# Performance work log

Hardware: AMD Instinct MI355X
Metric: run time of the kernel (lower is better)

The kernel has to match this reference:

```python
import jax, jax.numpy as jnp
import numpy as np

CONF_THRES = 0.2   # from __init__ default
IOU_THRES = 0.6    # from __init__ default
MAX_WH = 4096.0    # class-offset for multi-class NMS (yolov7 convention)
TOPK = 2048        # pre-NMS candidates per image
MAX_DET = 300      # max detections per image (yolov7 default)
B, N, NC = 8, 25200, 80


def setup_inputs() -> dict:
    key = jax.random.key(0)
    k1, k2, k3 = jax.random.split(key, 3)
    # decoded predictions: [cx, cy, w, h, obj, cls_0..cls_79]
    xywh = jax.random.uniform(k1, (B, N, 4)) * jnp.array([640.0, 640.0, 120.0, 120.0])
    obj = jax.random.uniform(k2, (B, N, 1))
    cls = jax.random.uniform(k3, (B, N, NC))
    preds = jnp.concatenate([xywh, obj, cls], axis=-1)  # [B, N, 85]
    return {"preds": preds}


def _xywh2xyxy(xywh):
    cx, cy, w, h = xywh[..., 0], xywh[..., 1], xywh[..., 2], xywh[..., 3]
    return jnp.stack([cx - w * 0.5, cy - h * 0.5, cx + w * 0.5, cy + h * 0.5], axis=-1)


def _box_iou(a, b):
    # a: [K,4], b: [K,4] -> [K,K] pairwise IoU
    area_a = (a[:, 2] - a[:, 0]) * (a[:, 3] - a[:, 1])
    area_b = (b[:, 2] - b[:, 0]) * (b[:, 3] - b[:, 1])
    lt = jnp.maximum(a[:, None, :2], b[None, :, :2])  # [K,K,2]
    rb = jnp.minimum(a[:, None, 2:], b[None, :, 2:])
    wh = jnp.clip(rb - lt, 0.0)
    inter = wh[..., 0] * wh[..., 1]
    return inter / (area_a[:, None] + area_b[None, :] - inter + 1e-9)


def _nms_single(pred):
    # pred: [N, 5+NC]
    boxes = _xywh2xyxy(pred[:, :4])                 # [N,4]
    scores_all = pred[:, 5:] * pred[:, 4:5]         # obj * cls  [N,NC]
    conf = jnp.max(scores_all, axis=-1)             # best-class conf
    cls_id = jnp.argmax(scores_all, axis=-1)
    scores = jnp.where(conf > CONF_THRES, conf, 0.0)

    # pre-NMS top-k candidates (sorted descending)
    top_scores, idx = jax.lax.top_k(scores, TOPK)
    top_boxes = boxes[idx]                          # [K,4]
    top_cls = cls_id[idx]                           # [K]
    top_valid = top_scores > CONF_THRES

    # per-class NMS via class offset so cross-class boxes never overlap
    offset_boxes = top_boxes + (top_cls.astype(top_boxes.dtype) * MAX_WH)[:, None]
    iou = _box_iou(offset_boxes, offset_boxes)      # [K,K]

    # greedy NMS over score-sorted candidates
    def body(i, state):
        keep, suppressed = state
        k_i = top_valid[i] & jnp.logical_not(suppressed[i])
        keep = keep.at[i].set(k_i)
        sup_new = suppressed | (k_i & (iou[i] > IOU_THRES))
        sup_new = sup_new.at[i].set(suppressed[i])  # never self-suppress
        return keep, sup_new

    keep, _ = jax.lax.fori_loop(
        0, TOPK, body,
        (jnp.zeros(TOPK, dtype=bool), jnp.zeros(TOPK, dtype=bool)))

    # take top MAX_DET kept detections
    keep_scores = jnp.where(keep, top_scores, -1.0)
    det_scores, det_idx = jax.lax.top_k(keep_scores, MAX_DET)
    det = jnp.concatenate(
        [top_boxes[det_idx],
         det_scores[:, None],
         top_cls[det_idx].astype(pred.dtype)[:, None]], axis=-1)  # [MAX_DET,6]
    det = jnp.where((det_scores > 0.0)[:, None], det, 0.0)
    return det


def reference(preds):
    # preds: [B, N, 5+NC] -> [B, MAX_DET, 6] (x1,y1,x2,y2,conf,cls), zero-padded
    return jax.vmap(_nms_single)(preds)
```

## Files before the change

### kernel.cpp

```cpp
#include <hip/hip_runtime.h>

#define BATCH 8
#define NPRED 25200
#define NCLS 80
#define ROWW 85
#define TOPKK 2048
#define MAXDET 300
#define CANDMAX 4096
#define NBUCKET 4096
#define CONF_T 0.2f
#define IOU_T 0.6f
#define CLS_OFF 4096.0f

#define MASKN 384
#define MCH (MASKN / 64)
#define MW 13

typedef unsigned long long u64;
typedef unsigned int u32;

__device__ __forceinline__ int bucket_of_key(u64 k) {
    float sc = __uint_as_float((u32)(k >> 32));
    int bkt = (int)(sc * (float)NBUCKET);
    return (bkt > NBUCKET - 1) ? (NBUCKET - 1) : bkt;
}

__global__ __launch_bounds__(256) void k_score(
    const float* __restrict__ preds,
    u64* __restrict__ keys,
    unsigned char* __restrict__ cls8)
{
    __shared__ float4 rows4[64 * ROWW / 4 + 4];
    const int t = threadIdx.x;
    const int lane = t & 63;
    const int wave = t >> 6;
    const size_t rowbase = (size_t)blockIdx.x * 64;
    const float4* src = reinterpret_cast<const float4*>(preds + rowbase * ROWW);

    for (int q = wave; q < 21; q += 4) {
        __builtin_amdgcn_global_load_lds(
            (const __attribute__((address_space(1))) void*)(src + q * 64 + lane),
            (__attribute__((address_space(3))) void*)(rows4 + q * 64),
            16, 0, 0);
    }
    if (t < 16) rows4[1344 + t] = src[1344 + t];
    __syncthreads();

    const float* rows = reinterpret_cast<const float*>(rows4);
    const int r = t >> 2;
    const int j = t & 3;
    const float* p = rows + r * ROWW;
    const float obj = p[4];

    float best = -1.0f;
    int bi = 0;
    #pragma unroll
    for (int tt = 0; tt < 20; ++tt) {
        int c = j + 4 * tt;
        float s = __fmul_rn(obj, p[5 + c]);
        if (s > best) { best = s; bi = c; }
    }
    #pragma unroll
    for (int d = 1; d <= 2; d <<= 1) {
        float os = __shfl_xor(best, d);
        int oi = __shfl_xor(bi, d);
        if (os > best || (os == best && oi < bi)) { best = os; bi = oi; }
    }

    if (j == 0) {
        unsigned gid = (unsigned)rowbase + r;
        u64 key = 0ull;
        if (best > CONF_T) {
            key = ((u64)__float_as_uint(best) << 32) | (0xFFFFFFFFu - (gid % NPRED));
        }
        keys[gid] = key;
        cls8[gid] = (unsigned char)bi;
    }
}

__global__ __launch_bounds__(1024) void k_scan(
    const u64* __restrict__ keys,
    u32* __restrict__ bstart_g,
    u32* __restrict__ balloc_g,
    int* __restrict__ tb_g,
    u32* __restrict__ stored_g)
{
    __shared__ u32 histL[NBUCKET];
    __shared__ u32 wtot[16];
    __shared__ u32 wsuf[16];
    __shared__ int s_tb;
    __shared__ u32 s_stored;

    const int b = blockIdx.x;
    const int t = threadIdx.x;
    const int lane = t & 63;
    const int wave = t >> 6;

    for (int i = t; i < NBUCKET; i += 1024) histL[i] = 0u;
    __syncthreads();

    const uint4* k4 = reinterpret_cast<const uint4*>(keys + (size_t)b * NPRED);
    for (int i = t; i < NPRED / 2; i += 1024) {
        uint4 v = k4[i];
        u64 ka = ((u64)v.y << 32) | v.x;
        u64 kb = ((u64)v.w << 32) | v.z;
        if (ka) atomicAdd(&histL[bucket_of_key(ka)], 1u);
        if (kb) atomicAdd(&histL[bucket_of_key(kb)], 1u);
    }
    __syncthreads();

    u32 h0 = histL[4 * t], h1 = histL[4 * t + 1], h2 = histL[4 * t + 2], h3 = histL[4 * t + 3];
    u32 ps = h0 + h1 + h2 + h3;

    u32 v = ps;
    #pragma unroll
    for (int off = 1; off < 64; off <<= 1) {
        u32 u2 = __shfl_down(v, off);
        if (lane + off < 64) v += u2;
    }
    if (lane == 0) wtot[wave] = v;
    __syncthreads();
    if (t < 16) {
        u32 w = wtot[t];
        u32 s = w;
        #pragma unroll
        for (int off = 1; off < 16; off <<= 1) {
            u32 u2 = __shfl_down(s, off);
            if (t + off < 16) s += u2;
        }
        wsuf[t] = s - w;
    }
    if (t == 0) s_tb = 0;
    __syncthreads();
    u32 suffix_t = v + wsuf[wave];
    u32 snext = suffix_t - ps;

    u32 b3 = snext;
    u32 b2 = b3 + h3;
    u32 b1 = b2 + h2;
    u32 b0 = b1 + h1;
    const size_t B0 = (size_t)b * NBUCKET;
    bstart_g[B0 + 4 * t + 0] = b0;
    bstart_g[B0 + 4 * t + 1] = b1;
    bstart_g[B0 + 4 * t + 2] = b2;
    bstart_g[B0 + 4 * t + 3] = b3;
    balloc_g[B0 + 4 * t + 0] = b0;
    balloc_g[B0 + 4 * t + 1] = b1;
    balloc_g[B0 + 4 * t + 2] = b2;
    balloc_g[B0 + 4 * t + 3] = b3;

    if (t == 0) s_stored = (suffix_t < (u32)CANDMAX) ? suffix_t : (u32)CANDMAX;
    __syncthreads();
    {
        u32 c3 = b3 + h3, c2 = b2 + h2, c1 = b1 + h1, c0 = b0 + h0;
        if (c3 >= TOPKK && b3 < TOPKK) { s_tb = 4 * t + 3; s_stored = (c3 < (u32)CANDMAX) ? c3 : (u32)CANDMAX; }
        if (c2 >= TOPKK && b2 < TOPKK) { s_tb = 4 * t + 2; s_stored = (c2 < (u32)CANDMAX) ? c2 : (u32)CANDMAX; }
        if (c1 >= TOPKK && b1 < TOPKK) { s_tb = 4 * t + 1; s_stored = (c1 < (u32)CANDMAX) ? c1 : (u32)CANDMAX; }
        if (c0 >= TOPKK && b0 < TOPKK) { s_tb = 4 * t + 0; s_stored = (c0 < (u32)CANDMAX) ? c0 : (u32)CANDMAX; }
    }
    __syncthreads();
    if (t == 0) { tb_g[b] = s_tb; stored_g[b] = s_stored; }
}

__global__ __launch_bounds__(256) void k_compact(
    const u64* __restrict__ keys,
    u32* __restrict__ balloc_g,
    const int* __restrict__ tb_g,
    u64* __restrict__ cand_g)
{
    unsigned i2 = blockIdx.x * 256 + threadIdx.x;
    if (i2 >= BATCH * NPRED / 2) return;
    uint4 v = reinterpret_cast<const uint4*>(keys)[i2];
    int b = (int)(i2 / (NPRED / 2));
    int tb = tb_g[b];
    u64 ka = ((u64)v.y << 32) | v.x;
    u64 kb = ((u64)v.w << 32) | v.z;
    if (ka) {
        int bkt = bucket_of_key(ka);
        if (bkt >= tb) {
            u32 slot = atomicAdd(&balloc_g[(size_t)b * NBUCKET + bkt], 1u);
            if (slot < CANDMAX) cand_g[(size_t)b * CANDMAX + slot] = ka;
        }
    }
    if (kb) {
        int bkt = bucket_of_key(kb);
        if (bkt >= tb) {
            u32 slot = atomicAdd(&balloc_g[(size_t)b * NBUCKET + bkt], 1u);
            if (slot < CANDMAX) cand_g[(size_t)b * CANDMAX + slot] = kb;
        }
    }
}

struct RankPhase {
    u32 bstartL[NBUCKET];
};
struct NmsPhase {
    u32 masks32[MASKN * MW];
    float4 cbx[MASKN];
    float carea[MASKN];
    float4 kb[MAXDET];
};

__global__ __launch_bounds__(1024) void k_finish(
    const float* __restrict__ preds,
    const unsigned char* __restrict__ cls8,
    const u32* __restrict__ bstart_g,
    const int* __restrict__ tb_g,
    const u32* __restrict__ stored_g,
    const u64* __restrict__ cand_g,
    float* __restrict__ out)
{
    __shared__ union { RankPhase rk; NmsPhase nms; } u;
    __shared__ u64 candL[CANDMAX];
    __shared__ unsigned short rank2cand[TOPKK];
    __shared__ float4 sbox[MASKN];
    __shared__ float sscore[MASKN];
    __shared__ float scls[MASKN];
    __shared__ u64 validw[MCH];

    const int b = blockIdx.x;
    const int t = threadIdx.x;
    const int lane = t & 63;
    const int wave = t >> 6;
    float* ob = out + (size_t)b * MAXDET * 6;
    const u32 stored = stored_g[b];
    const int tb = tb_g[b];
    const int tb2 = (tb > 0) ? tb - 1 : 0;

    for (int i = tb2 + t; i < NBUCKET; i += 1024)
        u.rk.bstartL[i] = bstart_g[(size_t)b * NBUCKET + i];
    for (int i = t; i < TOPKK; i += 1024) rank2cand[i] = 0xFFFFu;
    for (int i = t; i < CANDMAX; i += 1024)
        if ((u32)i < stored) candL[i] = cand_g[(size_t)b * CANDMAX + i];
    if (t < MASKN) {
        sbox[t] = make_float4(0.f, 0.f, 0.f, 0.f);
        sscore[t] = 0.f;
        scls[t] = 0.f;
    }
    __syncthreads();

    for (u32 i = t; i < stored; i += 1024) {
        u64 k = candL[i];
        int bkt = bucket_of_key(k);
        u32 base = u.rk.bstartL[bkt];
        u32 end = (bkt == 0) ? stored : u.rk.bstartL[bkt - 1];
        if (end > stored) end = stored;
        u32 r = base;
        for (u32 jx = base; jx < end; ++jx) r += (candL[jx] > k) ? 1u : 0u;
        if (r < TOPKK) rank2cand[r] = (unsigned short)i;
        if (r < MASKN) {
            float sc = __uint_as_float((u32)(k >> 32));
            unsigned idx = 0xFFFFFFFFu - (u32)(k & 0xFFFFFFFFu);
            const float* p = preds + ((size_t)b * NPRED + idx) * ROWW;
            float cx = p[0], cy = p[1], w = p[2], h = p[3];
            float hw = __fmul_rn(w, 0.5f);
            float hh = __fmul_rn(h, 0.5f);
            sbox[r] = make_float4(__fsub_rn(cx, hw), __fsub_rn(cy, hh),
                                  __fadd_rn(cx, hw), __fadd_rn(cy, hh));
            sscore[r] = sc;
            scls[r] = (float)cls8[(size_t)b * NPRED + idx];
        }
    }
    __syncthreads();

    if (t < MASKN) {
        float sc = sscore[t];
        float cl = scls[t];
        float4 bb = sbox[t];
        float off = __fmul_rn(cl, CLS_OFF);
        float4 obx = make_float4(__fadd_rn(bb.x, off), __fadd_rn(bb.y, off),
                                 __fadd_rn(bb.z, off), __fadd_rn(bb.w, off));
        u.nms.cbx[t] = obx;
        u.nms.carea[t] = __fmul_rn(__fsub_rn(obx.z, obx.x), __fsub_rn(obx.w, obx.y));
        u64 vb = __ballot(sc > CONF_T);
        if (lane == 0) validw[wave] = vb;
    }
    __syncthreads();

    for (int tu = 0; tu < 3; ++tu) {
        int uidx = wave + 16 * tu;
        if (uidx >= 42) break;
        int q, s;
        if (uidx < 12)      { q = 0; s = uidx; }
        else if (uidx < 22) { q = 1; s = uidx - 12 + 2; }
        else if (uidx < 30) { q = 2; s = uidx - 22 + 4; }
        else if (uidx < 36) { q = 3; s = uidx - 30 + 6; }
        else if (uidx < 40) { q = 4; s = uidx - 36 + 8; }
        else                { q = 5; s = uidx - 40 + 10; }

        const int r = q * 64 + lane;
        const float4 me = u.nms.cbx[r];
        const float aA = u.nms.carea[r];
        const int j0 = s * 32;
        u32 acc = 0u;
        #pragma unroll 8
        for (int jj = 0; jj < 32; ++jj) {
            const int jx = j0 + jj;
            float4 cb = u.nms.cbx[jx];
            float lx = fmaxf(me.x, cb.x), ly = fmaxf(me.y, cb.y);
            float rx = fminf(me.z, cb.z), ry = fminf(me.w, cb.w);
            float iw = fmaxf(__fsub_rn(rx, lx), 0.0f);
            float ih = fmaxf(__fsub_rn(ry, ly), 0.0f);
            float inter = __fmul_rn(iw, ih);
            float denom = __fadd_rn(__fsub_rn(__fadd_rn(aA, u.nms.carea[jx]), inter), 1e-9f);
            bool sv = inter > __fmul_rn(IOU_T, denom);
            acc |= ((u32)sv) << jj;
        }
        if (s == 2 * q || s == 2 * q + 1) {
            int shift = r - j0;
            u32 dm = (shift < 0) ? ~0u : ((shift >= 31) ? 0u : (~0u << (shift + 1)));
            acc &= dm;
        }
        u.nms.masks32[r * MW + s] = acc;
    }
    __syncthreads();
    if (wave != 0) return;

    const u64 below = (lane == 0) ? 0ull : (~0ull >> (64 - lane));
    u64 S[MCH];
    #pragma unroll
    for (int w = 0; w < MCH; ++w) S[w] = 0ull;
    int nk = 0;
    bool done = false, allfull = true;

    #pragma unroll
    for (int c = 0; c < MCH; ++c) {
        if (done) break;
        u64 vw = validw[c];
        u64 eligible = vw & ~S[c];
        const int rbase = (c * 64 + lane) * MW;
        u64 Mu = ((u64)u.nms.masks32[rbase + 2 * c + 1] << 32) |
                 (u64)u.nms.masks32[rbase + 2 * c];
        bool elig = (eligible >> lane) & 1ull;
        if (eligible) {
            int cap = MAXDET - nk;
            u64 edge = __ballot(elig && ((Mu & eligible) != 0ull));
            u64 keptm;
            if (edge == 0ull) {
                int rank = __popcll(eligible & below);
                keptm = __ballot(elig && (rank < cap));
            } else {
                u64 km = 0ull, supm = 0ull;
                int cnt = 0;
                for (int m = 0; m < 64 && cnt < cap; ++m) {
                    if (!((eligible >> m) & 1ull)) continue;
                    if ((supm >> m) & 1ull) continue;
                    km |= 1ull << m;
                    ++cnt;
                    supm |= __shfl(Mu, m);
                }
                keptm = km;
            }
            if ((keptm >> lane) & 1ull) {
                int pos = nk + __popcll(keptm & below);
                int i = c * 64 + lane;
                float4 bb = sbox[i];
                u.nms.kb[pos] = u.nms.cbx[i];
                float* row = ob + pos * 6;
                row[0] = bb.x; row[1] = bb.y; row[2] = bb.z; row[3] = bb.w;
                row[4] = sscore[i]; row[5] = scls[i];
            }
            nk += __popcll(keptm);
            if (nk >= MAXDET) {
                done = true;
            } else if (keptm) {
                for (int w = c + 1; w < MCH; ++w) {
                    u64 v2 = ((keptm >> lane) & 1ull)
                        ? (((u64)u.nms.masks32[rbase + 2 * w + 1] << 32) |
                           (u64)u.nms.masks32[rbase + 2 * w])
                        : 0ull;
                    v2 |= __shfl_xor(v2, 1);  v2 |= __shfl_xor(v2, 2);
                    v2 |= __shfl_xor(v2, 4);  v2 |= __shfl_xor(v2, 8);
                    v2 |= __shfl_xor(v2, 16); v2 |= __shfl_xor(v2, 32);
                    S[w] |= v2;
                }
            }
        }
        if (vw != ~0ull) { allfull = false; break; }
    }

    if (!done && allfull && nk < MAXDET) {
        __threadfence_block();
        for (int c = MCH; c < TOPKK / 64; ++c) {
            int r = c * 64 + lane;
            unsigned short ci = rank2cand[r];
            bool valid = (ci != 0xFFFFu);
            u64 validmask = __ballot(valid);
            if (validmask == 0ull) break;

            float sc = 0.f, cl = 0.f;
            float bx1 = 0.f, by1 = 0.f, bx2 = 0.f, by2 = 0.f;
            if (valid) {
                u64 k = candL[ci];
                sc = __uint_as_float((u32)(k >> 32));
                unsigned idx = 0xFFFFFFFFu - (u32)(k & 0xFFFFFFFFu);
                const float* p = preds + ((size_t)b * NPRED + idx) * ROWW;
                float cx = p[0], cy = p[1], w = p[2], h = p[3];
                float hw = __fmul_rn(w, 0.5f);
                float hh = __fmul_rn(h, 0.5f);
                bx1 = __fsub_rn(cx, hw); by1 = __fsub_rn(cy, hh);
                bx2 = __fadd_rn(cx, hw); by2 = __fadd_rn(cy, hh);
                cl = (float)cls8[(size_t)b * NPRED + idx];
            }
            float off = __fmul_rn(cl, CLS_OFF);
            float x1 = __fadd_rn(bx1, off), y1 = __fadd_rn(by1, off);
            float x2 = __fadd_rn(bx2, off), y2 = __fadd_rn(by2, off);
            float areaA = __fmul_rn(__fsub_rn(x2, x1), __fsub_rn(y2, y1));

            bool sup = false;
            for (int jx = 0; jx < nk; ++jx) {
                float4 k4 = u.nms.kb[jx];
                float lx = fmaxf(x1, k4.x), ly = fmaxf(y1, k4.y);
                float rx = fminf(x2, k4.z), ry = fminf(y2, k4.w);
                float iw = fmaxf(__fsub_rn(rx, lx), 0.0f);
                float ih = fmaxf(__fsub_rn(ry, ly), 0.0f);
                float inter = __fmul_rn(iw, ih);
                float areaB = __fmul_rn(__fsub_rn(k4.z, k4.x), __fsub_rn(k4.w, k4.y));
                float denom = __fadd_rn(__fsub_rn(__fadd_rn(areaA, areaB), inter), 1e-9f);
                if (inter > __fmul_rn(IOU_T, denom)) sup = true;
            }
            u64 supprev = __ballot(sup);

            u32 sb_lo = 0u, sb_hi = 0u;
            for (int m = 0; m < 64; ++m) {
                float mx1 = __shfl(x1, m), my1 = __shfl(y1, m);
                float mx2 = __shfl(x2, m), my2 = __shfl(y2, m);
                float lx = fmaxf(x1, mx1), ly = fmaxf(y1, my1);
                float rx = fminf(x2, mx2), ry = fminf(y2, my2);
                float iw = fmaxf(__fsub_rn(rx, lx), 0.0f);
                float ih = fmaxf(__fsub_rn(ry, ly), 0.0f);
                float inter = __fmul_rn(iw, ih);
                float areaB = __fmul_rn(__fsub_rn(mx2, mx1), __fsub_rn(my2, my1));
                float denom = __fadd_rn(__fsub_rn(__fadd_rn(areaA, areaB), inter), 1e-9f);
                bool s = (m != lane) && (inter > __fmul_rn(IOU_T, denom));
                if (m < 32) sb_lo |= ((u32)s) << m;
                else        sb_hi |= ((u32)s) << (m - 32);
            }

            u64 eligible = validmask & ~supprev;
            u64 mysb = (((u64)sb_hi << 32) | (u64)sb_lo);
            bool iselig = (eligible >> lane) & 1ull;
            u64 edgeball = __ballot(iselig && ((mysb & eligible & below) != 0ull));

            u64 keptm;
            int cap = MAXDET - nk;
            if (edgeball == 0ull) {
                int rank = __popcll(eligible & below);
                keptm = __ballot(iselig && (rank < cap));
            } else {
                u64 km = 0ull;
                int cnt = 0;
                for (int m = 0; m < 64 && cnt < cap; ++m) {
                    if (!((validmask >> m) & 1ull)) break;
                    if ((supprev >> m) & 1ull) continue;
                    u32 mlo = (u32)__shfl((int)sb_lo, m);
                    u32 mhi = (u32)__shfl((int)sb_hi, m);
                    u64 supby = (((u64)mhi << 32) | (u64)mlo);
                    if (supby & km) continue;
                    km |= 1ull << m;
                    ++cnt;
                }
                keptm = km;
            }

            if ((keptm >> lane) & 1ull) {
                int pos = nk + __popcll(keptm & below);
                u.nms.kb[pos] = make_float4(x1, y1, x2, y2);
                float* row = ob + pos * 6;
                row[0] = bx1; row[1] = by1; row[2] = bx2; row[3] = by2;
                row[4] = sc;  row[5] = cl;
            }
            __threadfence_block();
            nk += __popcll(keptm);
            if (nk >= MAXDET) break;
            if (validmask != ~0ull) break;
        }
    }

    for (int x = nk * 6 + lane; x < MAXDET * 6; x += 64) ob[x] = 0.0f;
}

extern "C" void kernel_launch(void* const* d_in, const int* in_sizes, int n_in,
                              void* d_out, int out_size, void* d_ws, size_t ws_size,
                              hipStream_t stream) {
    const float* preds = (const float*)d_in[0];
    float* out = (float*)d_out;

    u64* keys     = (u64*)d_ws;
    u64* cand_g   = keys + (size_t)BATCH * NPRED;
    u32* bstart_g = (u32*)(cand_g + (size_t)BATCH * CANDMAX);
    u32* balloc_g = bstart_g + BATCH * NBUCKET;
    int* tb_g     = (int*)(balloc_g + BATCH * NBUCKET);
    u32* stored_g = (u32*)(tb_g + 8);
    unsigned char* cls8 = (unsigned char*)(stored_g + 8);

    hipLaunchKernelGGL(k_score, dim3(BATCH * NPRED / 64), dim3(256), 0, stream,
                       preds, keys, cls8);
    hipLaunchKernelGGL(k_scan, dim3(BATCH), dim3(1024), 0, stream,
                       keys, bstart_g, balloc_g, tb_g, stored_g);
    hipLaunchKernelGGL(k_compact, dim3((BATCH * NPRED / 2 + 255) / 256), dim3(256), 0, stream,
                       keys, balloc_g, tb_g, cand_g);
    hipLaunchKernelGGL(k_finish, dim3(BATCH), dim3(1024), 0, stream,
                       preds, cls8, bstart_g, tb_g, stored_g, cand_g, out);
}
```

Measured before the change: 56.01 us.

## Fuse score, scan, compact and NMS stages into one cooperative kernel

Replaces the four separate launches (score, histogram scan, compaction, finish/NMS) with a single cooperative kernel of 256 blocks × 1024 threads, separated by grid-wide syncs. The scoring stage now loops over row tiles inside each persistent block and uses 16 threads per row instead of 4. The goal is to remove inter-kernel launch gaps and the idle time between stages. The trade-offs are three grid barriers, one tile of loads in flight per block with a block sync per tile (which can cut memory-level parallelism on the bandwidth-heavy scoring pass), and a large shared-memory union that limits occupancy.

```diff
diff --git a/kernel.cpp b/kernel.cpp
--- a/kernel.cpp
+++ b/kernel.cpp
@@ -1,4 +1,7 @@
 #include <hip/hip_runtime.h>
+#include <hip/hip_cooperative_groups.h>
+
+namespace cg = cooperative_groups;
 
 #define BATCH 8
 #define NPRED 25200
@@ -15,6 +18,9 @@
 #define MASKN 384
 #define MCH (MASKN / 64)
 #define MW 13
+#define NTILE (BATCH * NPRED / 64)
+#define GRID 256
+#define BLK 1024
 
 typedef unsigned long long u64;
 typedef unsigned int u32;
@@ -25,459 +31,456 @@
     return (bkt > NBUCKET - 1) ? (NBUCKET - 1) : bkt;
 }
 
-__global__ __launch_bounds__(256) void k_score(
+struct FinishLDS {
+    union {
+        u32 bstartL[NBUCKET];
+        struct {
+            u32 masks32[MASKN * MW];
+            float4 cbx[MASKN];
+            float carea[MASKN];
+            float4 kb[MAXDET];
+        } nms;
+    } v;
+    u64 candL[CANDMAX];
+    unsigned short rank2cand[TOPKK];
+    float4 sbox[MASKN];
+    float sscore[MASKN];
+    float scls[MASKN];
+    u64 validw[MCH];
+};
+
+__global__ __launch_bounds__(BLK) void k_mega(
     const float* __restrict__ preds,
     u64* __restrict__ keys,
-    unsigned char* __restrict__ cls8)
-{
-    __shared__ float4 rows4[64 * ROWW / 4 + 4];
-    const int t = threadIdx.x;
-    const int lane = t & 63;
-    const int wave = t >> 6;
-    const size_t rowbase = (size_t)blockIdx.x * 64;
-    const float4* src = reinterpret_cast<const float4*>(preds + rowbase * ROWW);
-
-    for (int q = wave; q < 21; q += 4) {
-        __builtin_amdgcn_global_load_lds(
-            (const __attribute__((address_space(1))) void*)(src + q * 64 + lane),
-            (__attribute__((address_space(3))) void*)(rows4 + q * 64),
-            16, 0, 0);
-    }
-    if (t < 16) rows4[1344 + t] = src[1344 + t];
-    __syncthreads();
-
-    const float* rows = reinterpret_cast<const float*>(rows4);
-    const int r = t >> 2;
-    const int j = t & 3;
-    const float* p = rows + r * ROWW;
-    const float obj = p[4];
-
-    float best = -1.0f;
-    int bi = 0;
-    #pragma unroll
-    for (int tt = 0; tt < 20; ++tt) {
-        int c = j + 4 * tt;
-        float s = __fmul_rn(obj, p[5 + c]);
-        if (s > best) { best = s; bi = c; }
-    }
-    #pragma unroll
-    for (int d = 1; d <= 2; d <<= 1) {
-        float os = __shfl_xor(best, d);
-        int oi = __shfl_xor(bi, d);
-        if (os > best || (os == best && oi < bi)) { best = os; bi = oi; }
-    }
-
-    if (j == 0) {
-        unsigned gid = (unsigned)rowbase + r;
-        u64 key = 0ull;
-        if (best > CONF_T) {
-            key = ((u64)__float_as_uint(best) << 32) | (0xFFFFFFFFu - (gid % NPRED));
-        }
-        keys[gid] = key;
-        cls8[gid] = (unsigned char)bi;
-    }
-}
-
-__global__ __launch_bounds__(1024) void k_scan(
-    const u64* __restrict__ keys,
+    unsigned char* __restrict__ cls8,
     u32* __restrict__ bstart_g,
     u32* __restrict__ balloc_g,
     int* __restrict__ tb_g,
-    u32* __restrict__ stored_g)
+    u32* __restrict__ stored_g,
+    u64* __restrict__ cand_g,
+    float* __restrict__ out)
 {
-    __shared__ u32 histL[NBUCKET];
+    __shared__ union {
+        float4 rows4[1364];
+        u32 histL[NBUCKET];
+        FinishLDS fin;
+    } L;
     __shared__ u32 wtot[16];
     __shared__ u32 wsuf[16];
     __shared__ int s_tb;
     __shared__ u32 s_stored;
 
-    const int b = blockIdx.x;
+    cg::grid_group grid = cg::this_grid();
+    const int bid = blockIdx.x;
     const int t = threadIdx.x;
     const int lane = t & 63;
     const int wave = t >> 6;
 
-    for (int i = t; i < NBUCKET; i += 1024) histL[i] = 0u;
-    __syncthreads();
-
-    const uint4* k4 = reinterpret_cast<const uint4*>(keys + (size_t)b * NPRED);
-    for (int i = t; i < NPRED / 2; i += 1024) {
-        uint4 v = k4[i];
-        u64 ka = ((u64)v.y << 32) | v.x;
-        u64 kb = ((u64)v.w << 32) | v.z;
-        if (ka) atomicAdd(&histL[bucket_of_key(ka)], 1u);
-        if (kb) atomicAdd(&histL[bucket_of_key(kb)], 1u);
+    for (int tile = bid; tile < NTILE; tile += GRID) {
+        const size_t rowbase = (size_t)tile * 64;
+        const float4* src = reinterpret_cast<const float4*>(preds + rowbase * ROWW);
+        for (int q = wave; q < 21; q += 16) {
+            __builtin_amdgcn_global_load_lds(
+                (const __attribute__((address_space(1))) void*)(src + q * 64 + lane),
+                (__attribute__((address_space(3))) void*)(L.rows4 + q * 64),
+                16, 0, 0);
+        }
+        if (t < 16) L.rows4[1344 + t] = src[1344 + t];
+        __syncthreads();
+
+        const float* rows = reinterpret_cast<const float*>(L.rows4);
+        const int r = t >> 4;
+        const int j = t & 15;
+        const float* p = rows + r * ROWW;
+        const float obj = p[4];
+
+        float best = -1.0f;
+        int bi = 0;
+        #pragma unroll
+        for (int tt = 0; tt < 5; ++tt) {
+            int c = j + 16 * tt;
+            float s = __fmul_rn(obj, p[5 + c]);
+            if (s > best) { best = s; bi = c; }
+        }
+        #pragma unroll
+        for (int d = 1; d <= 8; d <<= 1) {
+            float os = __shfl_xor(best, d);
+            int oi = __shfl_xor(bi, d);
+            if (os > best || (os == best && oi < bi)) { best = os; bi = oi; }
+        }
+
+        if (j == 0) {
+            unsigned gid = (unsigned)rowbase + r;
+            u64 key = 0ull;
+            if (best > CONF_T) {
+                key = ((u64)__float_as_uint(best) << 32) | (0xFFFFFFFFu - (gid % NPRED));
+            }
+            keys[gid] = key;
+            cls8[gid] = (unsigned char)bi;
+        }
+        __syncthreads();
     }
-    __syncthreads();
-
-    u32 h0 = histL[4 * t], h1 = histL[4 * t + 1], h2 = histL[4 * t + 2], h3 = histL[4 * t + 3];
-    u32 ps = h0 + h1 + h2 + h3;
-
-    u32 v = ps;
-    #pragma unroll
-    for (int off = 1; off < 64; off <<= 1) {
-        u32 u2 = __shfl_down(v, off);
-        if (lane + off < 64) v += u2;
+
+    grid.sync();
+
+    if (bid < BATCH) {
+        const int b = bid;
+        for (int i = t; i < NBUCKET; i += BLK) L.histL[i] = 0u;
+        __syncthreads();
+
+        const uint4* k4 = reinterpret_cast<const uint4*>(keys + (size_t)b * NPRED);
+        for (int i = t; i < NPRED / 2; i += BLK) {
+            uint4 v = k4[i];
+            u64 ka = ((u64)v.y << 32) | v.x;
+            u64 kb = ((u64)v.w << 32) | v.z;
+            if (ka) atomicAdd(&L.histL[bucket_of_key(ka)], 1u);
+            if (kb) atomicAdd(&L.histL[bucket_of_key(kb)], 1u);
+        }
+        __syncthreads();
+
+        u32 h0 = L.histL[4 * t], h1 = L.histL[4 * t + 1];
+        u32 h2 = L.histL[4 * t + 2], h3 = L.histL[4 * t + 3];
+        u32 ps = h0 + h1 + h2 + h3;
+
+        u32 v = ps;
+        #pragma unroll
+        for (int off = 1; off < 64; off <<= 1) {
+            u32 u2 = __shfl_down(v, off);
+            if (lane + off < 64) v += u2;
+        }
+        if (lane == 0) wtot[wave] = v;
+        __syncthreads();
+        if (t < 16) {
+            u32 w = wtot[t];
+            u32 s = w;
+            #pragma unroll
+            for (int off = 1; off < 16; off <<= 1) {
+                u32 u2 = __shfl_down(s, off);
+                if (t + off < 16) s += u2;
+            }
+            wsuf[t] = s - w;
+        }
+        if (t == 0) s_tb = 0;
+        __syncthreads();
+        u32 suffix_t = v + wsuf[wave];
+        u32 snext = suffix_t - ps;
+
+        u32 b3 = snext;
+        u32 b2 = b3 + h3;
+        u32 b1 = b2 + h2;
+        u32 b0 = b1 + h1;
+        const size_t B0 = (size_t)b * NBUCKET;
+        bstart_g[B0 + 4 * t + 0] = b0;
+        bstart_g[B0 + 4 * t + 1] = b1;
+        bstart_g[B0 + 4 * t + 2] = b2;
+        bstart_g[B0 + 4 * t + 3] = b3;
+        balloc_g[B0 + 4 * t + 0] = b0;
+        balloc_g[B0 + 4 * t + 1] = b1;
+        balloc_g[B0 + 4 * t + 2] = b2;
+        balloc_g[B0 + 4 * t + 3] = b3;
+
+        if (t == 0) s_stored = (suffix_t < (u32)CANDMAX) ? suffix_t : (u32)CANDMAX;
+        __syncthreads();
+        {
+            u32 c3 = b3 + h3, c2 = b2 + h2, c1 = b1 + h1, c0 = b0 + h0;
+            if (c3 >= TOPKK && b3 < TOPKK) { s_tb = 4 * t + 3; s_stored = (c3 < (u32)CANDMAX) ? c3 : (u32)CANDMAX; }
+            if (c2 >= TOPKK && b2 < TOPKK) { s_tb = 4 * t + 2; s_stored = (c2 < (u32)CANDMAX) ? c2 : (u32)CANDMAX; }
+            if (c1 >= TOPKK && b1 < TOPKK) { s_tb = 4 * t + 1; s_stored = (c1 < (u32)CANDMAX) ? c1 : (u32)CANDMAX; }
+            if (c0 >= TOPKK && b0 < TOPKK) { s_tb = 4 * t + 0; s_stored = (c0 < (u32)CANDMAX) ? c0 : (u32)CANDMAX; }
+        }
+        __syncthreads();
+        if (t == 0) { tb_g[b] = s_tb; stored_g[b] = s_stored; }
     }
-    if (lane == 0) wtot[wave] = v;
-    __syncthreads();
-    if (t < 16) {
-        u32 w = wtot[t];
-        u32 s = w;
-        #pragma unroll
-        for (int off = 1; off < 16; off <<= 1) {
-            u32 u2 = __shfl_down(s, off);
-            if (t + off < 16) s += u2;
-        }
-        wsuf[t] = s - w;
+
+    grid.sync();
+
+    {
+        unsigned i2 = bid * BLK + t;
+        if (i2 < BATCH * NPRED / 2) {
+            uint4 v = reinterpret_cast<const uint4*>(keys)[i2];
+            int b = (int)(i2 / (NPRED / 2));
+            int tb = tb_g[b];
+            u64 ka = ((u64)v.y << 32) | v.x;
+            u64 kb = ((u64)v.w << 32) | v.z;
+            if (ka) {
+                int bkt = bucket_of_key(ka);
+                if (bkt >= tb) {
+                    u32 slot = atomicAdd(&balloc_g[(size_t)b * NBUCKET + bkt], 1u);
+                    if (slot < CANDMAX) cand_g[(size_t)b * CANDMAX + slot] = ka;
+                }
+            }
+            if (kb) {
+                int bkt = bucket_of_key(kb);
+                if (bkt >= tb) {
+                    u32 slot = atomicAdd(&balloc_g[(size_t)b * NBUCKET + bkt], 1u);
+                    if (slot < CANDMAX) cand_g[(size_t)b * CANDMAX + slot] = kb;
+                }
+            }
+        }
     }
-    if (t == 0) s_tb = 0;
-    __syncthreads();
-    u32 suffix_t = v + wsuf[wave];
-    u32 snext = suffix_t - ps;
-
-    u32 b3 = snext;
-    u32 b2 = b3 + h3;
-    u32 b1 = b2 + h2;
-    u32 b0 = b1 + h1;
-    const size_t B0 = (size_t)b * NBUCKET;
-    bstart_g[B0 + 4 * t + 0] = b0;
-    bstart_g[B0 + 4 * t + 1] = b1;
-    bstart_g[B0 + 4 * t + 2] = b2;
-    bstart_g[B0 + 4 * t + 3] = b3;
-    balloc_g[B0 + 4 * t + 0] = b0;
-    balloc_g[B0 + 4 * t + 1] = b1;
-    balloc_g[B0 + 4 * t + 2] = b2;
-    balloc_g[B0 + 4 * t + 3] = b3;
-
-    if (t == 0) s_stored = (suffix_t < (u32)CANDMAX) ? suffix_t : (u32)CANDMAX;
-    __syncthreads();
+
+    grid.sync();
+
+    if (bid >= BATCH) return;
     {
-        u32 c3 = b3 + h3, c2 = b2 + h2, c1 = b1 + h1, c0 = b0 + h0;
-        if (c3 >= TOPKK && b3 < TOPKK) { s_tb = 4 * t + 3; s_stored = (c3 < (u32)CANDMAX) ? c3 : (u32)CANDMAX; }
-        if (c2 >= TOPKK && b2 < TOPKK) { s_tb = 4 * t + 2; s_stored = (c2 < (u32)CANDMAX) ? c2 : (u32)CANDMAX; }
-        if (c1 >= TOPKK && b1 < TOPKK) { s_tb = 4 * t + 1; s_stored = (c1 < (u32)CANDMAX) ? c1 : (u32)CANDMAX; }
-        if (c0 >= TOPKK && b0 < TOPKK) { s_tb = 4 * t + 0; s_stored = (c0 < (u32)CANDMAX) ? c0 : (u32)CANDMAX; }
-    }
-    __syncthreads();
-    if (t == 0) { tb_g[b] = s_tb; stored_g[b] = s_stored; }
-}
-
-__global__ __launch_bounds__(256) void k_compact(
-    const u64* __restrict__ keys,
-    u32* __restrict__ balloc_g,
-    const int* __restrict__ tb_g,
-    u64* __restrict__ cand_g)
-{
-    unsigned i2 = blockIdx.x * 256 + threadIdx.x;
-    if (i2 >= BATCH * NPRED / 2) return;
-    uint4 v = reinterpret_cast<const uint4*>(keys)[i2];
-    int b = (int)(i2 / (NPRED / 2));
-    int tb = tb_g[b];
-    u64 ka = ((u64)v.y << 32) | v.x;
-    u64 kb = ((u64)v.w << 32) | v.z;
-    if (ka) {
-        int bkt = bucket_of_key(ka);
-        if (bkt >= tb) {
-            u32 slot = atomicAdd(&balloc_g[(size_t)b * NBUCKET + bkt], 1u);
-            if (slot < CANDMAX) cand_g[(size_t)b * CANDMAX + slot] = ka;
-        }
-    }
-    if (kb) {
-        int bkt = bucket_of_key(kb);
-        if (bkt >= tb) {
-            u32 slot = atomicAdd(&balloc_g[(size_t)b * NBUCKET + bkt], 1u);
-            if (slot < CANDMAX) cand_g[(size_t)b * CANDMAX + slot] = kb;
-        }
-    }
-}
-
-struct RankPhase {
-    u32 bstartL[NBUCKET];
-};
-struct NmsPhase {
-    u32 masks32[MASKN * MW];
-    float4 cbx[MASKN];
-    float carea[MASKN];
-    float4 kb[MAXDET];
-};
-
-__global__ __launch_bounds__(1024) void k_finish(
-    const float* __restrict__ preds,
-    const unsigned char* __restrict__ cls8,
-    const u32* __restrict__ bstart_g,
-    const int* __restrict__ tb_g,
-    const u32* __restrict__ stored_g,
-    const u64* __restrict__ cand_g,
-    float* __restrict__ out)
-{
-    __shared__ union { RankPhase rk; NmsPhase nms; } u;
-    __shared__ u64 candL[CANDMAX];
-    __shared__ unsigned short rank2cand[TOPKK];
-    __shared__ float4 sbox[MASKN];
-    __shared__ float sscore[MASKN];
-    __shared__ float scls[MASKN];
-    __shared__ u64 validw[MCH];
-
-    const int b = blockIdx.x;
-    const int t = threadIdx.x;
-    const int lane = t & 63;
-    const int wave = t >> 6;
-    float* ob = out + (size_t)b * MAXDET * 6;
-    const u32 stored = stored_g[b];
-    const int tb = tb_g[b];
-    const int tb2 = (tb > 0) ? tb - 1 : 0;
-
-    for (int i = tb2 + t; i < NBUCKET; i += 1024)
-        u.rk.bstartL[i] = bstart_g[(size_t)b * NBUCKET + i];
-    for (int i = t; i < TOPKK; i += 1024) rank2cand[i] = 0xFFFFu;
-    for (int i = t; i < CANDMAX; i += 1024)
-        if ((u32)i < stored) candL[i] = cand_g[(size_t)b * CANDMAX + i];
-    if (t < MASKN) {
-        sbox[t] = make_float4(0.f, 0.f, 0.f, 0.f);
-        sscore[t] = 0.f;
-        scls[t] = 0.f;
-    }
-    __syncthreads();
-
-    for (u32 i = t; i < stored; i += 1024) {
-        u64 k = candL[i];
-        int bkt = bucket_of_key(k);
-        u32 base = u.rk.bstartL[bkt];
-        u32 end = (bkt == 0) ? stored : u.rk.bstartL[bkt - 1];
-        if (end > stored) end = stored;
-        u32 r = base;
-        for (u32 jx = base; jx < end; ++jx) r += (candL[jx] > k) ? 1u : 0u;
-        if (r < TOPKK) rank2cand[r] = (unsigned short)i;
-        if (r < MASKN) {
-            float sc = __uint_as_float((u32)(k >> 32));
-            unsigned idx = 0xFFFFFFFFu - (u32)(k & 0xFFFFFFFFu);
-            const float* p = preds + ((size_t)b * NPRED + idx) * ROWW;
-            float cx = p[0], cy = p[1], w = p[2], h = p[3];
-            float hw = __fmul_rn(w, 0.5f);
-            float hh = __fmul_rn(h, 0.5f);
-            sbox[r] = make_float4(__fsub_rn(cx, hw), __fsub_rn(cy, hh),
-                                  __fadd_rn(cx, hw), __fadd_rn(cy, hh));
-            sscore[r] = sc;
-            scls[r] = (float)cls8[(size_t)b * NPRED + idx];
-        }
-    }
-    __syncthreads();
-
-    if (t < MASKN) {
-        float sc = sscore[t];
-        float cl = scls[t];
-        float4 bb = sbox[t];
-        float off = __fmul_rn(cl, CLS_OFF);
-        float4 obx = make_float4(__fadd_rn(bb.x, off), __fadd_rn(bb.y, off),
-                                 __fadd_rn(bb.z, off), __fadd_rn(bb.w, off));
-        u.nms.cbx[t] = obx;
-        u.nms.carea[t] = __fmul_rn(__fsub_rn(obx.z, obx.x), __fsub_rn(obx.w, obx.y));
-        u64 vb = __ballot(sc > CONF_T);
-        if (lane == 0) validw[wave] = vb;
-    }
-    __syncthreads();
-
-    for (int tu = 0; tu < 3; ++tu) {
-        int uidx = wave + 16 * tu;
-        if (uidx >= 42) break;
-        int q, s;
-        if (uidx < 12)      { q = 0; s = uidx; }
-        else if (uidx < 22) { q = 1; s = uidx - 12 + 2; }
-        else if (uidx < 30) { q = 2; s = uidx - 22 + 4; }
-        else if (uidx < 36) { q = 3; s = uidx - 30 + 6; }
-        else if (uidx < 40) { q = 4; s = uidx - 36 + 8; }
-        else                { q = 5; s = uidx - 40 + 10; }
-
-        const int r = q * 64 + lane;
-        const float4 me = u.nms.cbx[r];
-        const float aA = u.nms.carea[r];
-        const int j0 = s * 32;
-        u32 acc = 0u;
-        #pragma unroll 8
-        for (int jj = 0; jj < 32; ++jj) {
-            const int jx = j0 + jj;
-            float4 cb = u.nms.cbx[jx];
-            float lx = fmaxf(me.x, cb.x), ly = fmaxf(me.y, cb.y);
-            float rx = fminf(me.z, cb.z), ry = fminf(me.w, cb.w);
-            float iw = fmaxf(__fsub_rn(rx, lx), 0.0f);
-            float ih = fmaxf(__fsub_rn(ry, ly), 0.0f);
-            float inter = __fmul_rn(iw, ih);
-            float denom = __fadd_rn(__fsub_rn(__fadd_rn(aA, u.nms.carea[jx]), inter), 1e-9f);
-            bool sv = inter > __fmul_rn(IOU_T, denom);
-            acc |= ((u32)sv) << jj;
-        }
-        if (s == 2 * q || s == 2 * q + 1) {
-            int shift = r - j0;
-            u32 dm = (shift < 0) ? ~0u : ((shift >= 31) ? 0u : (~0u << (shift + 1)));
-            acc &= dm;
-        }
-        u.nms.masks32[r * MW + s] = acc;
-    }
-    __syncthreads();
-    if (wave != 0) return;
-
-    const u64 below = (lane == 0) ? 0ull : (~0ull >> (64 - lane));
-    u64 S[MCH];
-    #pragma unroll
-    for (int w = 0; w < MCH; ++w) S[w] = 0ull;
-    int nk = 0;
-    bool done = false, allfull = true;
-
-    #pragma unroll
-    for (int c = 0; c < MCH; ++c) {
-        if (done) break;
-        u64 vw = validw[c];
-        u64 eligible = vw & ~S[c];
-        const int rbase = (c * 64 + lane) * MW;
-        u64 Mu = ((u64)u.nms.masks32[rbase + 2 * c + 1] << 32) |
-                 (u64)u.nms.masks32[rbase + 2 * c];
-        bool elig = (eligible >> lane) & 1ull;
-        if (eligible) {
-            int cap = MAXDET - nk;
-            u64 edge = __ballot(elig && ((Mu & eligible) != 0ull));
-            u64 keptm;
-            if (edge == 0ull) {
-                int rank = __popcll(eligible & below);
-                keptm = __ballot(elig && (rank < cap));
-            } else {
-                u64 km = 0ull, supm = 0ull;
-                int cnt = 0;
-                for (int m = 0; m < 64 && cnt < cap; ++m) {
-                    if (!((eligible >> m) & 1ull)) continue;
-                    if ((supm >> m) & 1ull) continue;
-                    km |= 1ull << m;
-                    ++cnt;
-                    supm |= __shfl(Mu, m);
-                }
-                keptm = km;
-            }
-            if ((keptm >> lane) & 1ull) {
-                int pos = nk + __popcll(keptm & below);
-                int i = c * 64 + lane;
-                float4 bb = sbox[i];
-                u.nms.kb[pos] = u.nms.cbx[i];
-                float* row = ob + pos * 6;
-                row[0] = bb.x; row[1] = bb.y; row[2] = bb.z; row[3] = bb.w;
-                row[4] = sscore[i]; row[5] = scls[i];
-            }
-            nk += __popcll(keptm);
-            if (nk >= MAXDET) {
-                done = true;
-            } else if (keptm) {
-                for (int w = c + 1; w < MCH; ++w) {
-                    u64 v2 = ((keptm >> lane) & 1ull)
-                        ? (((u64)u.nms.masks32[rbase + 2 * w + 1] << 32) |
-                           (u64)u.nms.masks32[rbase + 2 * w])
-                        : 0ull;
-                    v2 |= __shfl_xor(v2, 1);  v2 |= __shfl_xor(v2, 2);
-                    v2 |= __shfl_xor(v2, 4);  v2 |= __shfl_xor(v2, 8);
-                    v2 |= __shfl_xor(v2, 16); v2 |= __shfl_xor(v2, 32);
-                    S[w] |= v2;
-                }
-            }
-        }
-        if (vw != ~0ull) { allfull = false; break; }
-    }
-
-    if (!done && allfull && nk < MAXDET) {
-        __threadfence_block();
-        for (int c = MCH; c < TOPKK / 64; ++c) {
-            int r = c * 64 + lane;
-            unsigned short ci = rank2cand[r];
-            bool valid = (ci != 0xFFFFu);
-            u64 validmask = __ballot(valid);
-            if (validmask == 0ull) break;
-
-            float sc = 0.f, cl = 0.f;
-            float bx1 = 0.f, by1 = 0.f, bx2 = 0.f, by2 = 0.f;
-            if (valid) {
-                u64 k = candL[ci];
-                sc = __uint_as_float((u32)(k >> 32));
+        const int b = bid;
+        float* ob = out + (size_t)b * MAXDET * 6;
+        const u32 stored = stored_g[b];
+        const int tb = tb_g[b];
+        const int tb2 = (tb > 0) ? tb - 1 : 0;
+
+        for (int i = tb2 + t; i < NBUCKET; i += BLK)
+            L.fin.v.bstartL[i] = bstart_g[(size_t)b * NBUCKET + i];
+        for (int i = t; i < TOPKK; i += BLK) L.fin.rank2cand[i] = 0xFFFFu;
+        for (int i = t; i < CANDMAX; i += BLK)
+            if ((u32)i < stored) L.fin.candL[i] = cand_g[(size_t)b * CANDMAX + i];
+        if (t < MASKN) {
+            L.fin.sbox[t] = make_float4(0.f, 0.f, 0.f, 0.f);
+            L.fin.sscore[t] = 0.f;
+            L.fin.scls[t] = 0.f;
+        }
+        __syncthreads();
+
+        for (u32 i = t; i < stored; i += BLK) {
+            u64 k = L.fin.candL[i];
+            int bkt = bucket_of_key(k);
+            u32 base = L.fin.v.bstartL[bkt];
+            u32 end = (bkt == 0) ? stored : L.fin.v.bstartL[bkt - 1];
+            if (end > stored) end = stored;
+            u32 r = base;
+            for (u32 jx = base; jx < end; ++jx) r += (L.fin.candL[jx] > k) ? 1u : 0u;
+            if (r < TOPKK) L.fin.rank2cand[r] = (unsigned short)i;
+            if (r < MASKN) {
+                float sc = __uint_as_float((u32)(k >> 32));
                 unsigned idx = 0xFFFFFFFFu - (u32)(k & 0xFFFFFFFFu);
                 const float* p = preds + ((size_t)b * NPRED + idx) * ROWW;
                 float cx = p[0], cy = p[1], w = p[2], h = p[3];
                 float hw = __fmul_rn(w, 0.5f);
                 float hh = __fmul_rn(h, 0.5f);
-                bx1 = __fsub_rn(cx, hw); by1 = __fsub_rn(cy, hh);
-                bx2 = __fadd_rn(cx, hw); by2 = __fadd_rn(cy, hh);
-                cl = (float)cls8[(size_t)b * NPRED + idx];
-            }
+                L.fin.sbox[r] = make_float4(__fsub_rn(cx, hw), __fsub_rn(cy, hh),
+                                            __fadd_rn(cx, hw), __fadd_rn(cy, hh));
+                L.fin.sscore[r] = sc;
+                L.fin.scls[r] = (float)cls8[(size_t)b * NPRED + idx];
+            }
+        }
+        __syncthreads();
+
+        if (t < MASKN) {
+            float sc = L.fin.sscore[t];
+            float cl = L.fin.scls[t];
+            float4 bb = L.fin.sbox[t];
             float off = __fmul_rn(cl, CLS_OFF);
-            float x1 = __fadd_rn(bx1, off), y1 = __fadd_rn(by1, off);
-            float x2 = __fadd_rn(bx2, off), y2 = __fadd_rn(by2, off);
-            float areaA = __fmul_rn(__fsub_rn(x2, x1), __fsub_rn(y2, y1));
-
-            bool sup = false;
-            for (int jx = 0; jx < nk; ++jx) {
-                float4 k4 = u.nms.kb[jx];
-                float lx = fmaxf(x1, k4.x), ly = fmaxf(y1, k4.y);
-                float rx = fminf(x2, k4.z), ry = fminf(y2, k4.w);
+            float4 obx = make_float4(__fadd_rn(bb.x, off), __fadd_rn(bb.y, off),
+                                     __fadd_rn(bb.z, off), __fadd_rn(bb.w, off));
+            L.fin.v.nms.cbx[t] = obx;
+            L.fin.v.nms.carea[t] = __fmul_rn(__fsub_rn(obx.z, obx.x), __fsub_rn(obx.w, obx.y));
+            u64 vb = __ballot(sc > CONF_T);
+            if (lane == 0) L.fin.validw[wave] = vb;
+        }
+        __syncthreads();
+
+        for (int tu = 0; tu < 3; ++tu) {
+            int uidx = wave + 16 * tu;
+            if (uidx >= 42) break;
+            int q, s;
+            if (uidx < 12)      { q = 0; s = uidx; }
+            else if (uidx < 22) { q = 1; s = uidx - 12 + 2; }
+            else if (uidx < 30) { q = 2; s = uidx - 22 + 4; }
+            else if (uidx < 36) { q = 3; s = uidx - 30 + 6; }
+            else if (uidx < 40) { q = 4; s = uidx - 36 + 8; }
+            else                { q = 5; s = uidx - 40 + 10; }
+
+            const int r = q * 64 + lane;
+            const float4 me = L.fin.v.nms.cbx[r];
+            const float aA = L.fin.v.nms.carea[r];
+            const int j0 = s * 32;
+            u32 acc = 0u;
+            #pragma unroll 8
+            for (int jj = 0; jj < 32; ++jj) {
+                const int jx = j0 + jj;
+                float4 cb = L.fin.v.nms.cbx[jx];
+                float lx = fmaxf(me.x, cb.x), ly = fmaxf(me.y, cb.y);
+                float rx = fminf(me.z, cb.z), ry = fminf(me.w, cb.w);
                 float iw = fmaxf(__fsub_rn(rx, lx), 0.0f);
                 float ih = fmaxf(__fsub_rn(ry, ly), 0.0f);
                 float inter = __fmul_rn(iw, ih);
-                float areaB = __fmul_rn(__fsub_rn(k4.z, k4.x), __fsub_rn(k4.w, k4.y));
-                float denom = __fadd_rn(__fsub_rn(__fadd_rn(areaA, areaB), inter), 1e-9f);
-                if (inter > __fmul_rn(IOU_T, denom)) sup = true;
-            }
-            u64 supprev = __ballot(sup);
-
-            u32 sb_lo = 0u, sb_hi = 0u;
-            for (int m = 0; m < 64; ++m) {
-                float mx1 = __shfl(x1, m), my1 = __shfl(y1, m);
-                float mx2 = __shfl(x2, m), my2 = __shfl(y2, m);
-                float lx = fmaxf(x1, mx1), ly = fmaxf(y1, my1);
-                float rx = fminf(x2, mx2), ry = fminf(y2, my2);
-                float iw = fmaxf(__fsub_rn(rx, lx), 0.0f);
-                float ih = fmaxf(__fsub_rn(ry, ly), 0.0f);
-                float inter = __fmul_rn(iw, ih);
-                float areaB = __fmul_rn(__fsub_rn(mx2, mx1), __fsub_rn(my2, my1));
-                float denom = __fadd_rn(__fsub_rn(__fadd_rn(areaA, areaB), inter), 1e-9f);
-                bool s = (m != lane) && (inter > __fmul_rn(IOU_T, denom));
-                if (m < 32) sb_lo |= ((u32)s) << m;
-                else        sb_hi |= ((u32)s) << (m - 32);
-            }
-
-            u64 eligible = validmask & ~supprev;
-            u64 mysb = (((u64)sb_hi << 32) | (u64)sb_lo);
-            bool iselig = (eligible >> lane) & 1ull;
-            u64 edgeball = __ballot(iselig && ((mysb & eligible & below) != 0ull));
-
-            u64 keptm;
-            int cap = MAXDET - nk;
-            if (edgeball == 0ull) {
-                int rank = __popcll(eligible & below);
-                keptm = __ballot(iselig && (rank < cap));
-            } else {
-                u64 km = 0ull;
-                int cnt = 0;
-                for (int m = 0; m < 64 && cnt < cap; ++m) {
-                    if (!((validmask >> m) & 1ull)) break;
-                    if ((supprev >> m) & 1ull) continue;
-                    u32 mlo = (u32)__shfl((int)sb_lo, m);
-                    u32 mhi = (u32)__shfl((int)sb_hi, m);
-                    u64 supby = (((u64)mhi << 32) | (u64)mlo);
-                    if (supby & km) continue;
-                    km |= 1ull << m;
-                    ++cnt;
-                }
-                keptm = km;
-            }
-
-            if ((keptm >> lane) & 1ull) {
-                int pos = nk + __popcll(keptm & below);
-                u.nms.kb[pos] = make_float4(x1, y1, x2, y2);
-                float* row = ob + pos * 6;
-                row[0] = bx1; row[1] = by1; row[2] = bx2; row[3] = by2;
-                row[4] = sc;  row[5] = cl;
-            }
+                float denom = __fadd_rn(__fsub_rn(__fadd_rn(aA, L.fin.v.nms.carea[jx]), inter), 1e-9f);
+                bool sv = inter > __fmul_rn(IOU_T, denom);
+                acc |= ((u32)sv) << jj;
+            }
+            if (s == 2 * q || s == 2 * q + 1) {
+                int shift = r - j0;
+                u32 dm = (shift < 0) ? ~0u : ((shift >= 31) ? 0u : (~0u << (shift + 1)));
+                acc &= dm;
+            }
+            L.fin.v.nms.masks32[r * MW + s] = acc;
+        }
+        __syncthreads();
+        if (wave != 0) return;
+
+        const u64 below = (lane == 0) ? 0ull : (~0ull >> (64 - lane));
+        u64 S[MCH];
+        #pragma unroll
+        for (int w = 0; w < MCH; ++w) S[w] = 0ull;
+        int nk = 0;
+        bool done = false, allfull = true;
+
+        #pragma unroll
+        for (int c = 0; c < MCH; ++c) {
+            if (done) break;
+            u64 vw = L.fin.validw[c];
+            u64 eligible = vw & ~S[c];
+            const int rbase = (c * 64 + lane) * MW;
+            u64 Mu = ((u64)L.fin.v.nms.masks32[rbase + 2 * c + 1] << 32) |
+                     (u64)L.fin.v.nms.masks32[rbase + 2 * c];
+            bool elig = (eligible >> lane) & 1ull;
+            if (eligible) {
+                int cap = MAXDET - nk;
+                u64 edge = __ballot(elig && ((Mu & eligible) != 0ull));
+                u64 keptm;
+                if (edge == 0ull) {
+                    int rank = __popcll(eligible & below);
+                    keptm = __ballot(elig && (rank < cap));
+                } else {
+                    u64 km = 0ull, supm = 0ull;
+                    int cnt = 0;
+                    for (int m = 0; m < 64 && cnt < cap; ++m) {
+                        if (!((eligible >> m) & 1ull)) continue;
+                        if ((supm >> m) & 1ull) continue;
+                        km |= 1ull << m;
+                        ++cnt;
+                        supm |= __shfl(Mu, m);
+                    }
+                    keptm = km;
+                }
+                if ((keptm >> lane) & 1ull) {
+                    int pos = nk + __popcll(keptm & below);
+                    int i = c * 64 + lane;
+                    float4 bb = L.fin.sbox[i];
+                    L.fin.v.nms.kb[pos] = L.fin.v.nms.cbx[i];
+                    float* row = ob + pos * 6;
+                    row[0] = bb.x; row[1] = bb.y; row[2] = bb.z; row[3] = bb.w;
+                    row[4] = L.fin.sscore[i]; row[5] = L.fin.scls[i];
+                }
+                nk += __popcll(keptm);
+                if (nk >= MAXDET) {
+                    done = true;
+                } else if (keptm) {
+                    for (int w = c + 1; w < MCH; ++w) {
+                        u64 v2 = ((keptm >> lane) & 1ull)
+                            ? (((u64)L.fin.v.nms.masks32[rbase + 2 * w + 1] << 32) |
+                               (u64)L.fin.v.nms.masks32[rbase + 2 * w])
+                            : 0ull;
+                        v2 |= __shfl_xor(v2, 1);  v2 |= __shfl_xor(v2, 2);
+                        v2 |= __shfl_xor(v2, 4);  v2 |= __shfl_xor(v2, 8);
+                        v2 |= __shfl_xor(v2, 16); v2 |= __shfl_xor(v2, 32);
+                        S[w] |= v2;
+                    }
+                }
+            }
+            if (vw != ~0ull) { allfull = false; break; }
+        }
+
+        if (!done && allfull && nk < MAXDET) {
             __threadfence_block();
-            nk += __popcll(keptm);
-            if (nk >= MAXDET) break;
-            if (validmask != ~0ull) break;
-        }
+            for (int c = MCH; c < TOPKK / 64; ++c) {
+                int r = c * 64 + lane;
+                unsigned short ci = L.fin.rank2cand[r];
+                bool valid = (ci != 0xFFFFu);
+                u64 validmask = __ballot(valid);
+                if (validmask == 0ull) break;
+
+                float sc = 0.f, cl = 0.f;
+                float bx1 = 0.f, by1 = 0.f, bx2 = 0.f, by2 = 0.f;
+                if (valid) {
+                    u64 k = L.fin.candL[ci];
+                    sc = __uint_as_float((u32)(k >> 32));
+                    unsigned idx = 0xFFFFFFFFu - (u32)(k & 0xFFFFFFFFu);
+                    const float* p = preds + ((size_t)b * NPRED + idx) * ROWW;
+                    float cx = p[0], cy = p[1], w = p[2], h = p[3];
+                    float hw = __fmul_rn(w, 0.5f);
+                    float hh = __fmul_rn(h, 0.5f);
+                    bx1 = __fsub_rn(cx, hw); by1 = __fsub_rn(cy, hh);
+                    bx2 = __fadd_rn(cx, hw); by2 = __fadd_rn(cy, hh);
+                    cl = (float)cls8[(size_t)b * NPRED + idx];
+                }
+                float off = __fmul_rn(cl, CLS_OFF);
+                float x1 = __fadd_rn(bx1, off), y1 = __fadd_rn(by1, off);
+                float x2 = __fadd_rn(bx2, off), y2 = __fadd_rn(by2, off);
+                float areaA = __fmul_rn(__fsub_rn(x2, x1), __fsub_rn(y2, y1));
+
+                bool sup = false;
+                for (int jx = 0; jx < nk; ++jx) {
+                    float4 k4 = L.fin.v.nms.kb[jx];
+                    float lx = fmaxf(x1, k4.x), ly = fmaxf(y1, k4.y);
+                    float rx = fminf(x2, k4.z), ry = fminf(y2, k4.w);
+                    float iw = fmaxf(__fsub_rn(rx, lx), 0.0f);
+                    float ih = fmaxf(__fsub_rn(ry, ly), 0.0f);
+                    float inter = __fmul_rn(iw, ih);
+                    float areaB = __fmul_rn(__fsub_rn(k4.z, k4.x), __fsub_rn(k4.w, k4.y));
+                    float denom = __fadd_rn(__fsub_rn(__fadd_rn(areaA, areaB), inter), 1e-9f);
+                    if (inter > __fmul_rn(IOU_T, denom)) sup = true;
+                }
+                u64 supprev = __ballot(sup);
+
+                u32 sb_lo = 0u, sb_hi = 0u;
+                for (int m = 0; m < 64; ++m) {
+                    float mx1 = __shfl(x1, m), my1 = __shfl(y1, m);
+                    float mx2 = __shfl(x2, m), my2 = __shfl(y2, m);
+                    float lx = fmaxf(x1, mx1), ly = fmaxf(y1, my1);
+                    float rx = fminf(x2, mx2), ry = fminf(y2, my2);
+                    float iw = fmaxf(__fsub_rn(rx, lx), 0.0f);
+                    float ih = fmaxf(__fsub_rn(ry, ly), 0.0f);
+                    float inter = __fmul_rn(iw, ih);
+                    float areaB = __fmul_rn(__fsub_rn(mx2, mx1), __fsub_rn(my2, my1));
+                    float denom = __fadd_rn(__fsub_rn(__fadd_rn(areaA, areaB), inter), 1e-9f);
+                    bool s = (m != lane) && (inter > __fmul_rn(IOU_T, denom));
+                    if (m < 32) sb_lo |= ((u32)s) << m;
+                    else        sb_hi |= ((u32)s) << (m - 32);
+                }
+
+                u64 eligible = validmask & ~supprev;
+                u64 mysb = (((u64)sb_hi << 32) | (u64)sb_lo);
+                bool iselig = (eligible >> lane) & 1ull;
+                u64 edgeball = __ballot(iselig && ((mysb & eligible & below) != 0ull));
+
+                u64 keptm;
+                int cap = MAXDET - nk;
+                if (edgeball == 0ull) {
+                    int rank = __popcll(eligible & below);
+                    keptm = __ballot(iselig && (rank < cap));
+                } else {
+                    u64 km = 0ull;
+                    int cnt = 0;
+                    for (int m = 0; m < 64 && cnt < cap; ++m) {
+                        if (!((validmask >> m) & 1ull)) break;
+                        if ((supprev >> m) & 1ull) continue;
+                        u32 mlo = (u32)__shfl((int)sb_lo, m);
+                        u32 mhi = (u32)__shfl((int)sb_hi, m);
+                        u64 supby = (((u64)mhi << 32) | (u64)mlo);
+                        if (supby & km) continue;
+                        km |= 1ull << m;
+                        ++cnt;
+                    }
+                    keptm = km;
+                }
+
+                if ((keptm >> lane) & 1ull) {
+                    int pos = nk + __popcll(keptm & below);
+                    L.fin.v.nms.kb[pos] = make_float4(x1, y1, x2, y2);
+                    float* row = ob + pos * 6;
+                    row[0] = bx1; row[1] = by1; row[2] = bx2; row[3] = by2;
+                    row[4] = sc;  row[5] = cl;
+                }
+                __threadfence_block();
+                nk += __popcll(keptm);
+                if (nk >= MAXDET) break;
+                if (validmask != ~0ull) break;
+            }
+        }
+
+        for (int x = nk * 6 + lane; x < MAXDET * 6; x += 64) ob[x] = 0.0f;
     }
-
-    for (int x = nk * 6 + lane; x < MAXDET * 6; x += 64) ob[x] = 0.0f;
 }
 
 extern "C" void kernel_launch(void* const* d_in, const int* in_sizes, int n_in,
@@ -494,12 +497,11 @@
     u32* stored_g = (u32*)(tb_g + 8);
     unsigned char* cls8 = (unsigned char*)(stored_g + 8);
 
-    hipLaunchKernelGGL(k_score, dim3(BATCH * NPRED / 64), dim3(256), 0, stream,
-                       preds, keys, cls8);
-    hipLaunchKernelGGL(k_scan, dim3(BATCH), dim3(1024), 0, stream,
-                       keys, bstart_g, balloc_g, tb_g, stored_g);
-    hipLaunchKernelGGL(k_compact, dim3((BATCH * NPRED / 2 + 255) / 256), dim3(256), 0, stream,
-                       keys, balloc_g, tb_g, cand_g);
-    hipLaunchKernelGGL(k_finish, dim3(BATCH), dim3(1024), 0, stream,
-                       preds, cls8, bstart_g, tb_g, stored_g, cand_g, out);
+    void* args[] = {
+        (void*)&preds, (void*)&keys, (void*)&cls8,
+        (void*)&bstart_g, (void*)&balloc_g, (void*)&tb_g,
+        (void*)&stored_g, (void*)&cand_g, (void*)&out
+    };
+    hipLaunchCooperativeKernel((const void*)k_mega, dim3(GRID), dim3(BLK),
+                               args, 0, stream);
 }
```

New measurement: 160.4 us. 186% more time.
